# Kernel tuning notes

Hardware: AMD Instinct MI355X
Metric: run time of the kernel (lower is better)

The kernel has to match this reference:

```python
import jax, jax.numpy as jnp
import numpy as np

B, T, D, H, R = 4, 4096, 1024, 16, 256
DH = D // H  # 64


def setup_inputs() -> dict:
    key = jax.random.key(0)
    ks = jax.random.split(key, 5)
    s = 0.02
    return {
        "x": jax.random.normal(ks[0], (B, T, D), dtype=jnp.float32),
        "Wq": jax.random.normal(ks[1], (D, D), dtype=jnp.float32) * s,
        "bq": jnp.zeros((D,), dtype=jnp.float32),
        "Wd": jax.random.normal(ks[2], (D, R), dtype=jnp.float32) * s,
        "bd": jnp.zeros((R,), dtype=jnp.float32),
        "Wu": jax.random.normal(ks[3], (R, 2 * D), dtype=jnp.float32) * s,
        "bu": jnp.zeros((2 * D,), dtype=jnp.float32),
        "Wo": jax.random.normal(ks[4], (D, D), dtype=jnp.float32) * s,
        "bo": jnp.zeros((D,), dtype=jnp.float32),
    }


def reference(x, Wq, bq, Wd, bd, Wu, bu, Wo, bo):
    b, t = x.shape[0], x.shape[1]
    # q projection -> (B,T,H,DH)
    q = (x @ Wq + bq).reshape(b, t, H, DH)
    # low-rank KV: down then up -> (B,T,H,2*DH)
    kv = ((x @ Wd + bd) @ Wu + bu).reshape(b, t, H, 2 * DH)
    k, v = kv[..., :DH], kv[..., DH:]
    # elu+1 feature map
    q = jax.nn.elu(q) + 1.0
    k = jax.nn.elu(k) + 1.0
    # linear attention: context = k^T v per head -> (B,H,DH,DH)
    context = jnp.einsum("bthd,bthe->bhde", k, v)
    out = jnp.einsum("bthd,bhde->bthe", q, context)  # (B,T,H,DH)
    # normalizer: q . sum_t(k)
    k_sum = k.sum(axis=1)  # (B,H,DH)
    z = 1.0 / (jnp.einsum("bthd,bhd->bth", q, k_sum) + 1e-6)
    out = out * z[..., None]
    return out.reshape(b, t, D) @ Wo + bo
```

## Files before the change

### kernel.cpp

```cpp
#include <hip/hip_runtime.h>
#include <hip/hip_bf16.h>
#include <cstddef>
#include <cstdint>

#define B_  4
#define T_  4096
#define D_  1024
#define H_  16
#define DH_ 64
#define R_  256
#define BT_ (B_ * T_)
#define TWO_D_ (2 * D_)

typedef __attribute__((ext_vector_type(8))) short short8;
typedef __attribute__((ext_vector_type(4))) float f32x4;

__device__ __forceinline__ float elu1(float x) {
    return x > 0.0f ? x + 1.0f : __expf(x);
}

__device__ __forceinline__ float bf2f(short u) {
    union { uint32_t i; float f; } c;
    c.i = ((uint32_t)(uint16_t)u) << 16;
    return c.f;
}

typedef __attribute__((address_space(1))) void void_g;
typedef __attribute__((address_space(3))) void void_l;
__device__ __forceinline__ void gld_lds16(const void* g, void* l) {
    __builtin_amdgcn_global_load_lds(
        (const void_g*)(uintptr_t)g,
        (void_l*)(uint32_t)(uintptr_t)l,
        16, 0, 0);
}

__device__ __forceinline__ void store_out(float* p, float v) { *p = v; }
__device__ __forceinline__ void store_out(__hip_bfloat16* p, float v) { *p = __float2bfloat16(v); }

#define PBM 256
#define PBN 256
#define PBK 32

template<int EPI, bool BROW, typename OT>
__global__ __launch_bounds__(512, 2) void gemm_p2(
    const __hip_bfloat16* __restrict__ A,
    const __hip_bfloat16* __restrict__ Bt,
    const float* __restrict__ bias,
    OT* __restrict__ C,
    int M, int N, int K)
{
    __shared__ alignas(16) __hip_bfloat16 sm[2 * 4 * PBM * PBK];
    __hip_bfloat16* Asm = sm;
    __hip_bfloat16* Bsm = sm + 4 * PBM * PBK;

    const int nbx = N / PBN;
    const int nbm = M / PBM;
    const int sh = (nbm < 8) ? nbm : 8;
    const int id = blockIdx.x;
    const int strip = id / (sh * nbx);
    const int wi = id % (sh * nbx);
    const int bm = (strip * sh + (wi % sh)) * PBM;
    const int bn = (wi / sh) * PBN;

    const int tid  = threadIdx.x;
    const int lane = tid & 63;
    const int w    = tid >> 6;
    const int wm   = w >> 2;
    const int wn   = w & 3;
    const int r15  = lane & 15;
    const int kg   = lane >> 4;

    const int c0 = tid, c1 = tid + 512;
    const int rA0 = c0 >> 2, rA1 = c1 >> 2;
    const int gA0 = (c0 & 3) ^ (rA0 & 3), gA1 = (c1 & 3) ^ (rA1 & 3);
    const __hip_bfloat16* a0 = A  + (size_t)(bm + rA0) * K + gA0 * 8;
    const __hip_bfloat16* a1 = A  + (size_t)(bm + rA1) * K + gA1 * 8;
    const __hip_bfloat16* b0 = Bt + (size_t)(bn + rA0) * K + gA0 * 8;
    const __hip_bfloat16* b1 = Bt + (size_t)(bn + rA1) * K + gA1 * 8;

    auto stageA = [&](int t) {
        __hip_bfloat16* d = Asm + (t & 3) * (PBM * PBK);
        gld_lds16(a0 + t * PBK, d + c0 * 8);
        gld_lds16(a1 + t * PBK, d + c1 * 8);
    };
    auto stageB = [&](int t) {
        __hip_bfloat16* d = Bsm + (t & 3) * (PBM * PBK);
        gld_lds16(b0 + t * PBK, d + c0 * 8);
        gld_lds16(b1 + t * PBK, d + c1 * 8);
    };

    const int nk = K / PBK;
    f32x4 acc[8][4] = {};

    stageA(0); stageB(0); stageA(1); stageB(1);

    for (int kt = 0; kt < nk; ++kt) {
        const __hip_bfloat16* As_ = Asm + (kt & 3) * (PBM * PBK);
        const __hip_bfloat16* Bs_ = Bsm + (kt & 3) * (PBM * PBK);

        if (kt + 2 < nk) {
            stageA(kt + 2);
            asm volatile("s_waitcnt vmcnt(6)" ::: "memory");
        } else if (kt + 2 == nk) {
            asm volatile("s_waitcnt vmcnt(4)" ::: "memory");
        } else {
            asm volatile("s_waitcnt vmcnt(0)" ::: "memory");
        }
        __builtin_amdgcn_s_barrier();

        short8 af[8], bf[4];
#pragma unroll
        for (int i = 0; i < 4; ++i) {
            const int r = wm * 128 + i * 16 + r15;
            af[i] = *(const short8*)(As_ + r * PBK + ((kg ^ (r & 3)) * 8));
        }
#pragma unroll
        for (int j = 0; j < 4; ++j) {
            const int r = wn * 64 + j * 16 + r15;
            bf[j] = *(const short8*)(Bs_ + r * PBK + ((kg ^ (r & 3)) * 8));
        }
        __builtin_amdgcn_s_setprio(1);
#pragma unroll
        for (int i = 0; i < 4; ++i)
#pragma unroll
            for (int j = 0; j < 4; ++j)
                acc[i][j] = __builtin_amdgcn_mfma_f32_16x16x32_bf16(af[i], bf[j], acc[i][j], 0, 0, 0);
        __builtin_amdgcn_s_setprio(0);
        __builtin_amdgcn_s_barrier();

        if (kt + 2 < nk) stageB(kt + 2);
#pragma unroll
        for (int i = 4; i < 8; ++i) {
            const int r = wm * 128 + i * 16 + r15;
            af[i] = *(const short8*)(As_ + r * PBK + ((kg ^ (r & 3)) * 8));
        }
        __builtin_amdgcn_s_setprio(1);
#pragma unroll
        for (int i = 4; i < 8; ++i)
#pragma unroll
            for (int j = 0; j < 4; ++j)
                acc[i][j] = __builtin_amdgcn_mfma_f32_16x16x32_bf16(af[i], bf[j], acc[i][j], 0, 0, 0);
        __builtin_amdgcn_s_setprio(0);
        __builtin_amdgcn_s_barrier();
    }

    const int row0 = bm + wm * 128 + (lane >> 4) * 4;

    float brow[8][4];
    if (BROW) {
#pragma unroll
        for (int i = 0; i < 8; ++i)
#pragma unroll
            for (int r = 0; r < 4; ++r) brow[i][r] = bias[row0 + i * 16 + r];
    }
#pragma unroll
    for (int j = 0; j < 4; ++j) {
        const int col = bn + wn * 64 + j * 16 + r15;
        const float bv = BROW ? 0.0f : bias[col];
        const bool kp_col = ((col & 127) < 64);
#pragma unroll
        for (int i = 0; i < 8; ++i) {
#pragma unroll
            for (int r = 0; r < 4; ++r) {
                const int row = row0 + i * 16 + r;
                float v = acc[i][j][r] + (BROW ? brow[i][r] : bv);
                if (EPI == 1) v = elu1(v);
                else if (EPI == 2) {
                    const bool kp = BROW ? ((row & 127) < 64) : kp_col;
                    if (kp) v = elu1(v);
                }
                store_out(C + (size_t)row * N + col, v);
            }
        }
    }
}

#define BM 128
#define BN 128
#define BK 32
#define NBUF 5

template<int EPI, bool BROW, typename OT>
__global__ __launch_bounds__(256) void gemm_bf16(
    const __hip_bfloat16* __restrict__ A,
    const __hip_bfloat16* __restrict__ Bt,
    const float* __restrict__ bias,
    OT* __restrict__ C,
    OT* __restrict__ C2,
    int M, int N, int K)
{
    __shared__ alignas(16) __hip_bfloat16 As[NBUF * BM * BK];
    __shared__ alignas(16) __hip_bfloat16 Bs[NBUF * BN * BK];

    const int nbx = N / BN;
    const int id = blockIdx.x;
    const int strip = id / (8 * nbx);
    const int wi = id % (8 * nbx);
    const int bm = (strip * 8 + (wi & 7)) * BM;
    const int bn = (wi >> 3) * BN;

    const int tid  = threadIdx.x;
    const int lane = tid & 63;
    const int wm   = (tid >> 7) * 64;
    const int wn   = ((tid >> 6) & 1) * 64;
    const int r15  = lane & 15;
    const int kg   = lane >> 4;

    f32x4 acc[4][4] = {};

    const int c0 = tid, c1 = tid + 256;
    const __hip_bfloat16* a0 = A  + (size_t)(bm + (c0 >> 2)) * K + (c0 & 3) * 8;
    const __hip_bfloat16* a1 = A  + (size_t)(bm + (c1 >> 2)) * K + (c1 & 3) * 8;
    const __hip_bfloat16* b0 = Bt + (size_t)(bn + (c0 >> 2)) * K + (c0 & 3) * 8;
    const __hip_bfloat16* b1 = Bt + (size_t)(bn + (c1 >> 2)) * K + (c1 & 3) * 8;

    const int nk = K / BK;

    auto stage = [&](int t) {
        const int buf = t % NBUF;
        __hip_bfloat16* Ad = As + buf * (BM * BK);
        __hip_bfloat16* Bd = Bs + buf * (BN * BK);
        const int k0 = t * BK;
        gld_lds16(a0 + k0, Ad + c0 * 8);
        gld_lds16(a1 + k0, Ad + c1 * 8);
        gld_lds16(b0 + k0, Bd + c0 * 8);
        gld_lds16(b1 + k0, Bd + c1 * 8);
    };

    stage(0); stage(1); stage(2);

    for (int t = 0; t < nk; ++t) {
        if (t + 3 < nk) {
            stage(t + 3);
            asm volatile("s_waitcnt vmcnt(12)\ns_barrier" ::: "memory");
        } else if (t + 2 < nk) {
            asm volatile("s_waitcnt vmcnt(8)\ns_barrier" ::: "memory");
        } else if (t + 1 < nk) {
            asm volatile("s_waitcnt vmcnt(4)\ns_barrier" ::: "memory");
        } else {
            asm volatile("s_waitcnt vmcnt(0)\ns_barrier" ::: "memory");
        }

        const __hip_bfloat16* Asb = As + (t % NBUF) * (BM * BK);
        const __hip_bfloat16* Bsb = Bs + (t % NBUF) * (BN * BK);

        short8 af[4], bf[4];
#pragma unroll
        for (int i = 0; i < 4; ++i) {
            af[i] = *(const short8*)(Asb + (wm + i * 16 + r15) * BK + kg * 8);
            bf[i] = *(const short8*)(Bsb + (wn + i * 16 + r15) * BK + kg * 8);
        }
#pragma unroll
        for (int i = 0; i < 4; ++i)
#pragma unroll
            for (int j = 0; j < 4; ++j)
                acc[i][j] = __builtin_amdgcn_mfma_f32_16x16x32_bf16(af[i], bf[j], acc[i][j], 0, 0, 0);
    }

    const int row0 = bm + wm + (lane >> 4) * 4;

    if (EPI == 3) {
        const bool qreg = (bn < 1024);
#pragma unroll
        for (int j = 0; j < 4; ++j) {
            const int col = bn + wn + j * 16 + r15;
            const float bv = bias[col];
#pragma unroll
            for (int i = 0; i < 4; ++i)
#pragma unroll
                for (int r = 0; r < 4; ++r) {
                    const int row = row0 + i * 16 + r;
                    float v = acc[i][j][r] + bv;
                    if (qreg) {
                        store_out(C + (size_t)row * 1024 + col, elu1(v));
                    } else {
                        store_out(C2 + (size_t)row * 256 + (col - 1024), v);
                    }
                }
        }
        return;
    }

    float brow[4][4];
    if (BROW) {
#pragma unroll
        for (int i = 0; i < 4; ++i)
#pragma unroll
            for (int r = 0; r < 4; ++r) brow[i][r] = bias[row0 + i * 16 + r];
    }
#pragma unroll
    for (int j = 0; j < 4; ++j) {
        const int col = bn + wn + j * 16 + r15;
        const float bv = BROW ? 0.0f : bias[col];
        const bool kp_col = ((col & 127) < 64);
#pragma unroll
        for (int i = 0; i < 4; ++i) {
#pragma unroll
            for (int r = 0; r < 4; ++r) {
                const int row = row0 + i * 16 + r;
                float v = acc[i][j][r] + (BROW ? brow[i][r] : bv);
                if (EPI == 1) v = elu1(v);
                else if (EPI == 2) {
                    const bool kp = BROW ? ((row & 127) < 64) : kp_col;
                    if (kp) v = elu1(v);
                }
                store_out(C + (size_t)row * N + col, v);
            }
        }
    }
}

__global__ __launch_bounds__(256) void cast_bf16_kernel(
    const float* __restrict__ s, __hip_bfloat16* __restrict__ d, int n)
{
    const int i = (blockIdx.x * 256 + threadIdx.x) * 8;
    if (i >= n) return;
    float4 v0 = *(const float4*)(s + i);
    float4 v1 = *(const float4*)(s + i + 4);
    __hip_bfloat16 t[8];
    t[0] = __float2bfloat16(v0.x); t[1] = __float2bfloat16(v0.y);
    t[2] = __float2bfloat16(v0.z); t[3] = __float2bfloat16(v0.w);
    t[4] = __float2bfloat16(v1.x); t[5] = __float2bfloat16(v1.y);
    t[6] = __float2bfloat16(v1.z); t[7] = __float2bfloat16(v1.w);
    *(short8*)(d + i) = *(const short8*)t;
}

__global__ __launch_bounds__(256) void transpose_cast(
    const float* __restrict__ W, __hip_bfloat16* __restrict__ Wt, int K, int N)
{
    __shared__ float t[32][33];
    const int n0 = blockIdx.x * 32, k0 = blockIdx.y * 32;
    const int c = threadIdx.x & 31, r = threadIdx.x >> 5;
#pragma unroll
    for (int rr = r; rr < 32; rr += 8)
        t[rr][c] = W[(size_t)(k0 + rr) * N + n0 + c];
    __syncthreads();
#pragma unroll
    for (int rr = r; rr < 32; rr += 8)
        Wt[(size_t)(n0 + rr) * K + k0 + c] = __float2bfloat16(t[c][rr]);
}

#define CHT 512

__global__ __launch_bounds__(256) void ctx_mfma(
    const __hip_bfloat16* __restrict__ kvT, float* __restrict__ ctx,
    float* __restrict__ ksum)
{
    __shared__ alignas(16) unsigned char smem[40960];
    float* red0 = (float*)smem;
    float* red1 = (float*)(smem + 20480);

    const int bh = blockIdx.x >> 3;
    const int chunk = blockIdx.x & 7;
    const int b = bh >> 4;
    const int h = bh & 15;
    const int tid = threadIdx.x;
    const int lane = tid & 63;
    const int w = tid >> 6;
    const int r15 = lane & 15;
    const int kg  = lane >> 4;

    f32x4 acc[4][4] = {};
    f32x4 acc4[4] = {};

    const short one = (short)0x3F80;
    const short8 bfv = (r15 == 0)
        ? (short8){one, one, one, one, one, one, one, one}
        : (short8){0, 0, 0, 0, 0, 0, 0, 0};

    const size_t tbase = (size_t)b * T_ + (size_t)chunk * CHT;
    const __hip_bfloat16* src = kvT + (size_t)(h * 128) * BT_ + tbase;

    for (int it = 0; it < CHT / 128; ++it) {
#pragma unroll
        for (int r = 0; r < 8; ++r) {
            const int c = r * 256 + tid;
            const int s = c >> 9, j = (c >> 2) & 127, u = c & 3;
            gld_lds16(src + (size_t)j * BT_ + it * 128 + s * 32 + u * 8,
                      smem + c * 16);
        }
        __syncthreads();

        const __hip_bfloat16* Ls = (const __hip_bfloat16*)smem;
        short8 af[4], bf[4];
#pragma unroll
        for (int i = 0; i < 4; ++i) {
            af[i] = *(const short8*)(Ls + (w * 128 + i * 16 + r15) * 32 + kg * 8);
            bf[i] = *(const short8*)(Ls + (w * 128 + 64 + i * 16 + r15) * 32 + kg * 8);
        }
#pragma unroll
        for (int i = 0; i < 4; ++i) {
#pragma unroll
            for (int j = 0; j < 4; ++j)
                acc[i][j] = __builtin_amdgcn_mfma_f32_16x16x32_bf16(af[i], bf[j], acc[i][j], 0, 0, 0);
            acc4[i] = __builtin_amdgcn_mfma_f32_16x16x32_bf16(af[i], bfv, acc4[i], 0, 0, 0);
        }
        __syncthreads();
    }

    const int q4 = lane >> 4;
    auto wr = [&](float* reg) {
#pragma unroll
        for (int i = 0; i < 4; ++i) {
#pragma unroll
            for (int r = 0; r < 4; ++r) {
                const int row = i * 16 + q4 * 4 + r;
#pragma unroll
                for (int j = 0; j < 4; ++j) reg[row * 80 + j * 16 + r15] = acc[i][j][r];
                reg[row * 80 + 64 + r15] = acc4[i][r];
            }
        }
    };
    auto rd = [&](const float* reg) {
#pragma unroll
        for (int i = 0; i < 4; ++i) {
#pragma unroll
            for (int r = 0; r < 4; ++r) {
                const int row = i * 16 + q4 * 4 + r;
#pragma unroll
                for (int j = 0; j < 4; ++j) acc[i][j][r] += reg[row * 80 + j * 16 + r15];
                acc4[i][r] += reg[row * 80 + 64 + r15];
            }
        }
    };

    if (w == 1) wr(red0);
    if (w == 3) wr(red1);
    __syncthreads();
    if (w == 0) rd(red0);
    if (w == 2) rd(red1);
    __syncthreads();
    if (w == 2) wr(red0);
    __syncthreads();
    if (w == 0) { rd(red0); wr(red0); }
    __syncthreads();

    float* cdst = ctx + (size_t)bh * 4096;
#pragma unroll
    for (int r = 0; r < 16; ++r) {
        const int idx = r * 256 + tid;
        const int d = idx >> 6, e = idx & 63;
        atomicAdd(cdst + idx, red0[d * 80 + e]);
    }
    if (tid < 64) atomicAdd(ksum + bh * 64 + tid, red0[tid * 80 + 64]);
}

__global__ __launch_bounds__(256) void pack_ctx(
    const float* __restrict__ ctx, __hip_bfloat16* __restrict__ ctxT)
{
    __shared__ float L[64 * 65];
    const int bh = blockIdx.x;
    const int tid = threadIdx.x;
#pragma unroll
    for (int r = 0; r < 16; ++r) {
        const int idx = r * 256 + tid;
        L[(idx >> 6) * 65 + (idx & 63)] = ctx[(size_t)bh * 4096 + idx];
    }
    __syncthreads();
#pragma unroll
    for (int r = 0; r < 16; ++r) {
        const int idx = r * 256 + tid;
        ctxT[(size_t)bh * 4096 + idx] =
            __float2bfloat16(L[(idx & 63) * 65 + (idx >> 6)]);
    }
}

__global__ __launch_bounds__(256) void out_mfma(
    const __hip_bfloat16* __restrict__ qb, const __hip_bfloat16* __restrict__ ctxT,
    const float* __restrict__ ksum, __hip_bfloat16* __restrict__ outb)
{
    __shared__ alignas(16) unsigned char As[256 * 128];
    __shared__ alignas(16) unsigned char Bs[64 * 128];
    __shared__ float ksumL[64];
    __shared__ float zbuf[256];

    const int bh = blockIdx.x >> 4;
    const int tile = blockIdx.x & 15;
    const int b = bh >> 4;
    const int h = bh & 15;
    const int tid = threadIdx.x;
    const int lane = tid & 63;
    const int w = tid >> 6;
    const int r15 = lane & 15;
    const int kg  = lane >> 4;

    const size_t trow0 = (size_t)b * T_ + (size_t)tile * 256;

#pragma unroll
    for (int r = 0; r < 8; ++r) {
        const int c = r * 256 + tid;
        const int row = c >> 3, slot = c & 7, u = slot ^ (row & 7);
        gld_lds16(qb + (trow0 + row) * D_ + h * 64 + u * 8, As + c * 16);
    }
#pragma unroll
    for (int r = 0; r < 2; ++r) {
        const int c = r * 256 + tid;
        const int row = c >> 3, slot = c & 7, u = slot ^ (row & 7);
        gld_lds16(ctxT + (size_t)bh * 4096 + row * 64 + u * 8, Bs + c * 16);
    }
    if (tid < 64) ksumL[tid] = ksum[bh * 64 + tid];
    __syncthreads();

    short8 af[4][2], bf[4][2];
#pragma unroll
    for (int i = 0; i < 4; ++i)
#pragma unroll
        for (int s = 0; s < 2; ++s) {
            const int m = w * 64 + i * 16 + r15;
            const int n = i * 16 + r15;
            const int uk = s * 4 + kg;
            af[i][s] = *(const short8*)(As + m * 128 + ((uk ^ (m & 7)) * 16));
            bf[i][s] = *(const short8*)(Bs + n * 128 + ((uk ^ (n & 7)) * 16));
        }

    f32x4 acc[4][4] = {};
#pragma unroll
    for (int s = 0; s < 2; ++s)
#pragma unroll
        for (int i = 0; i < 4; ++i)
#pragma unroll
            for (int j = 0; j < 4; ++j)
                acc[i][j] = __builtin_amdgcn_mfma_f32_16x16x32_bf16(af[i][s], bf[j][s], acc[i][j], 0, 0, 0);

    float dsum[4];
#pragma unroll
    for (int i = 0; i < 4; ++i) {
        float s0 = 0.0f;
#pragma unroll
        for (int s = 0; s < 2; ++s)
#pragma unroll
            for (int j8 = 0; j8 < 8; ++j8)
                s0 += bf2f(af[i][s][j8]) * ksumL[s * 32 + kg * 8 + j8];
        s0 += __shfl_xor(s0, 16);
        s0 += __shfl_xor(s0, 32);
        dsum[i] = s0;
    }
    if (lane < 16) {
#pragma unroll
        for (int i = 0; i < 4; ++i)
            zbuf[w * 64 + i * 16 + lane] = 1.0f / (dsum[i] + 1e-6f);
    }
    __syncthreads();

    const int q4 = lane >> 4;
#pragma unroll
    for (int i = 0; i < 4; ++i) {
#pragma unroll
        for (int r = 0; r < 4; ++r) {
            const int m = w * 64 + i * 16 + q4 * 4 + r;
            const float z = zbuf[m];
#pragma unroll
            for (int j = 0; j < 4; ++j) {
                outb[(trow0 + m) * D_ + h * 64 + j * 16 + r15] =
                    __float2bfloat16(acc[i][j][r] * z);
            }
        }
    }
}

extern "C" void kernel_launch(void* const* d_in, const int* in_sizes, int n_in,
                              void* d_out, int out_size, void* d_ws, size_t ws_size,
                              hipStream_t stream) {
    const float* x  = (const float*)d_in[0];
    const float* Wq = (const float*)d_in[1];
    const float* bq = (const float*)d_in[2];
    const float* Wd = (const float*)d_in[3];
    const float* bd = (const float*)d_in[4];
    const float* Wu = (const float*)d_in[5];
    const float* bu = (const float*)d_in[6];
    const float* Wo = (const float*)d_in[7];
    const float* bo = (const float*)d_in[8];
    float* out = (float*)d_out;

    __hip_bfloat16* xb    = (__hip_bfloat16*)d_ws;
    __hip_bfloat16* WqdT  = xb    + (size_t)BT_ * D_;
    __hip_bfloat16* WuT   = WqdT  + (size_t)1280 * D_;
    __hip_bfloat16* WoT   = WuT   + (size_t)TWO_D_ * R_;
    __hip_bfloat16* xdb   = WoT   + (size_t)D_ * D_;
    __hip_bfloat16* kvT   = xdb   + (size_t)BT_ * R_;
    __hip_bfloat16* qb    = kvT   + (size_t)TWO_D_ * BT_;
    float* bias_qd = (float*)(qb + (size_t)BT_ * D_);
    float* ctx  = bias_qd + 1280;
    float* ksum = ctx + (size_t)B_ * H_ * DH_ * DH_;
    __hip_bfloat16* ctxT = (__hip_bfloat16*)(ksum + B_ * H_ * DH_);
    __hip_bfloat16* outb = xb;

    hipMemsetAsync(ctx, 0,
        (size_t)(B_ * H_ * DH_ * DH_ + B_ * H_ * DH_) * sizeof(float), stream);

    cast_bf16_kernel<<<(BT_ * D_) / (8 * 256), 256, 0, stream>>>(x, xb, BT_ * D_);
    transpose_cast<<<dim3(D_ / 32, D_ / 32), 256, 0, stream>>>(Wq, WqdT, D_, D_);
    transpose_cast<<<dim3(R_ / 32, D_ / 32), 256, 0, stream>>>(Wd, WqdT + (size_t)D_ * D_, D_, R_);
    transpose_cast<<<dim3(TWO_D_ / 32, R_ / 32), 256, 0, stream>>>(Wu, WuT, R_, TWO_D_);
    transpose_cast<<<dim3(D_ / 32, D_ / 32), 256, 0, stream>>>(Wo, WoT, D_, D_);

    gemm_bf16<0, false, __hip_bfloat16><<<(BT_ / BM) * (R_ / BN), 256, 0, stream>>>(
        xb, WqdT + (size_t)D_ * D_, bd, xdb, nullptr, BT_, R_, D_);
    gemm_p2<1, false, __hip_bfloat16><<<(BT_ / PBM) * (D_ / PBN), 512, 0, stream>>>(
        xb, WqdT, bq, qb, BT_, D_, D_);
    gemm_p2<2, true, __hip_bfloat16><<<(TWO_D_ / PBM) * (BT_ / PBN), 512, 0, stream>>>(
        WuT, xdb, bu, kvT, TWO_D_, BT_, R_);
    ctx_mfma<<<64 * (T_ / CHT), 256, 0, stream>>>(kvT, ctx, ksum);
    pack_ctx<<<64, 256, 0, stream>>>(ctx, ctxT);
    out_mfma<<<64 * 16, 256, 0, stream>>>(qb, ctxT, ksum, outb);
    gemm_p2<0, false, float><<<(BT_ / PBM) * (D_ / PBN), 512, 0, stream>>>(
        outb, WoT, bo, out, BT_, D_, D_);
}
```

Baseline: 336.1 us.

## Deepen GEMM LDS pipeline to three stages and prefetch next B fragments

```diff
diff --git a/kernel.cpp b/kernel.cpp
--- a/kernel.cpp
+++ b/kernel.cpp
@@ -72,7 +72,7 @@
 
     const int c0 = tid, c1 = tid + 512;
     const int rA0 = c0 >> 2, rA1 = c1 >> 2;
-    const int gA0 = (c0 & 3) ^ (rA0 & 3), gA1 = (c1 & 3) ^ (rA1 & 3);
+    const int gA0 = (c0 & 3) ^ ((rA0 >> 2) & 3), gA1 = (c1 & 3) ^ ((rA1 >> 2) & 3);
     const __hip_bfloat16* a0 = A  + (size_t)(bm + rA0) * K + gA0 * 8;
     const __hip_bfloat16* a1 = A  + (size_t)(bm + rA1) * K + gA1 * 8;
     const __hip_bfloat16* b0 = Bt + (size_t)(bn + rA0) * K + gA0 * 8;
@@ -91,57 +91,74 @@
 
     const int nk = K / PBK;
     f32x4 acc[8][4] = {};
-
-    stageA(0); stageB(0); stageA(1); stageB(1);
-
-    for (int kt = 0; kt < nk; ++kt) {
+    short8 bfA[4], bfB[4];
+
+    stageA(0); stageB(0); stageA(1); stageB(1); stageA(2); stageB(2);
+    asm volatile("s_waitcnt vmcnt(8)" ::: "memory");
+    __builtin_amdgcn_s_barrier();
+#pragma unroll
+    for (int j = 0; j < 4; ++j) {
+        const int r = wn * 64 + j * 16 + r15;
+        bfA[j] = *(const short8*)(Bsm + r * PBK + ((kg ^ ((r >> 2) & 3)) * 8));
+    }
+
+    auto step = [&](int kt, short8 (&bfc)[4], short8 (&bfn)[4]) {
         const __hip_bfloat16* As_ = Asm + (kt & 3) * (PBM * PBK);
-        const __hip_bfloat16* Bs_ = Bsm + (kt & 3) * (PBM * PBK);
-
-        if (kt + 2 < nk) {
-            stageA(kt + 2);
+        const __hip_bfloat16* Bn_ = Bsm + ((kt + 1) & 3) * (PBM * PBK);
+        short8 af0[4], af1[4];
+
+        if (kt + 3 < nk) stageA(kt + 3);
+#pragma unroll
+        for (int i = 0; i < 4; ++i) {
+            const int r = wm * 128 + i * 16 + r15;
+            af0[i] = *(const short8*)(As_ + r * PBK + ((kg ^ ((r >> 2) & 3)) * 8));
+        }
+#pragma unroll
+        for (int i = 0; i < 4; ++i) {
+            const int r = wm * 128 + 64 + i * 16 + r15;
+            af1[i] = *(const short8*)(As_ + r * PBK + ((kg ^ ((r >> 2) & 3)) * 8));
+        }
+        asm volatile("s_waitcnt lgkmcnt(4)" ::: "memory");
+        if (kt + 3 < nk) {
             asm volatile("s_waitcnt vmcnt(6)" ::: "memory");
-        } else if (kt + 2 == nk) {
+        } else if (kt + 2 < nk) {
             asm volatile("s_waitcnt vmcnt(4)" ::: "memory");
+        } else if (kt + 1 < nk) {
+            asm volatile("s_waitcnt vmcnt(0)" ::: "memory");
+        }
+        __builtin_amdgcn_s_barrier();
+        __builtin_amdgcn_s_setprio(1);
+#pragma unroll
+        for (int i = 0; i < 4; ++i)
+#pragma unroll
+            for (int j = 0; j < 4; ++j)
+                acc[i][j] = __builtin_amdgcn_mfma_f32_16x16x32_bf16(af0[i], bfc[j], acc[i][j], 0, 0, 0);
+        __builtin_amdgcn_s_setprio(0);
+
+        if (kt + 3 < nk) stageB(kt + 3);
+        if (kt + 1 < nk) {
+#pragma unroll
+            for (int j = 0; j < 4; ++j) {
+                const int r = wn * 64 + j * 16 + r15;
+                bfn[j] = *(const short8*)(Bn_ + r * PBK + ((kg ^ ((r >> 2) & 3)) * 8));
+            }
+            asm volatile("s_waitcnt lgkmcnt(4)" ::: "memory");
         } else {
-            asm volatile("s_waitcnt vmcnt(0)" ::: "memory");
+            asm volatile("s_waitcnt lgkmcnt(0)" ::: "memory");
         }
         __builtin_amdgcn_s_barrier();
-
-        short8 af[8], bf[4];
-#pragma unroll
-        for (int i = 0; i < 4; ++i) {
-            const int r = wm * 128 + i * 16 + r15;
-            af[i] = *(const short8*)(As_ + r * PBK + ((kg ^ (r & 3)) * 8));
-        }
-#pragma unroll
-        for (int j = 0; j < 4; ++j) {
-            const int r = wn * 64 + j * 16 + r15;
-            bf[j] = *(const short8*)(Bs_ + r * PBK + ((kg ^ (r & 3)) * 8));
-        }
         __builtin_amdgcn_s_setprio(1);
 #pragma unroll
         for (int i = 0; i < 4; ++i)
 #pragma unroll
             for (int j = 0; j < 4; ++j)
-                acc[i][j] = __builtin_amdgcn_mfma_f32_16x16x32_bf16(af[i], bf[j], acc[i][j], 0, 0, 0);
+                acc[4 + i][j] = __builtin_amdgcn_mfma_f32_16x16x32_bf16(af1[i], bfc[j], acc[4 + i][j], 0, 0, 0);
         __builtin_amdgcn_s_setprio(0);
-        __builtin_amdgcn_s_barrier();
-
-        if (kt + 2 < nk) stageB(kt + 2);
-#pragma unroll
-        for (int i = 4; i < 8; ++i) {
-            const int r = wm * 128 + i * 16 + r15;
-            af[i] = *(const short8*)(As_ + r * PBK + ((kg ^ (r & 3)) * 8));
-        }
-        __builtin_amdgcn_s_setprio(1);
-#pragma unroll
-        for (int i = 4; i < 8; ++i)
-#pragma unroll
-            for (int j = 0; j < 4; ++j)
-                acc[i][j] = __builtin_amdgcn_mfma_f32_16x16x32_bf16(af[i], bf[j], acc[i][j], 0, 0, 0);
-        __builtin_amdgcn_s_setprio(0);
-        __builtin_amdgcn_s_barrier();
+    };
+
+    for (int kt = 0; kt < nk; kt += 2) {
+        step(kt,     bfA, bfB);
+        step(kt + 1, bfB, bfA);
     }
 
     const int row0 = bm + wm * 128 + (lane >> 4) * 4;
```

After: 333.0 us. About the same (-0.9%).

## Rewrite 256x256 GEMM mainloop with BK=64 and 8-phase interleaved pipeline

Applied to the files above, without the earlier changes.

```diff
diff --git a/kernel.cpp b/kernel.cpp
--- a/kernel.cpp
+++ b/kernel.cpp
@@ -39,27 +39,25 @@
 
 #define PBM 256
 #define PBN 256
-#define PBK 32
 
 template<int EPI, bool BROW, typename OT>
-__global__ __launch_bounds__(512, 2) void gemm_p2(
+__global__ __launch_bounds__(512, 2) void gemm_p8(
     const __hip_bfloat16* __restrict__ A,
     const __hip_bfloat16* __restrict__ Bt,
     const float* __restrict__ bias,
     OT* __restrict__ C,
     int M, int N, int K)
 {
-    __shared__ alignas(16) __hip_bfloat16 sm[2 * 4 * PBM * PBK];
+    __shared__ alignas(16) __hip_bfloat16 sm[65536];
     __hip_bfloat16* Asm = sm;
-    __hip_bfloat16* Bsm = sm + 4 * PBM * PBK;
+    __hip_bfloat16* Bsm = sm + 32768;
 
     const int nbx = N / PBN;
     const int nbm = M / PBM;
     const int sh = (nbm < 8) ? nbm : 8;
     const int id = blockIdx.x;
-    const int strip = id / (sh * nbx);
     const int wi = id % (sh * nbx);
-    const int bm = (strip * sh + (wi % sh)) * PBM;
+    const int bm = ((id / (sh * nbx)) * sh + (wi % sh)) * PBM;
     const int bn = (wi / sh) * PBN;
 
     const int tid  = threadIdx.x;
@@ -70,79 +68,207 @@
     const int r15  = lane & 15;
     const int kg   = lane >> 4;
 
-    const int c0 = tid, c1 = tid + 512;
-    const int rA0 = c0 >> 2, rA1 = c1 >> 2;
-    const int gA0 = (c0 & 3) ^ (rA0 & 3), gA1 = (c1 & 3) ^ (rA1 & 3);
-    const __hip_bfloat16* a0 = A  + (size_t)(bm + rA0) * K + gA0 * 8;
-    const __hip_bfloat16* a1 = A  + (size_t)(bm + rA1) * K + gA1 * 8;
-    const __hip_bfloat16* b0 = Bt + (size_t)(bn + rA0) * K + gA0 * 8;
-    const __hip_bfloat16* b1 = Bt + (size_t)(bn + rA1) * K + gA1 * 8;
-
-    auto stageA = [&](int t) {
-        __hip_bfloat16* d = Asm + (t & 3) * (PBM * PBK);
-        gld_lds16(a0 + t * PBK, d + c0 * 8);
-        gld_lds16(a1 + t * PBK, d + c1 * 8);
+    const int nt = K / 64;
+
+    const int rl = tid >> 3;
+    const int g  = (tid & 7) ^ (rl & 7);
+    const __hip_bfloat16* aS = A  + (size_t)(bm + rl) * K + g * 8;
+    const __hip_bfloat16* bS = Bt + (size_t)(bn + rl) * K + g * 8;
+    __hip_bfloat16* dA = Asm + tid * 8;
+    __hip_bfloat16* dB = Bsm + tid * 8;
+
+    auto stA = [&](int t, int h) {
+        const int tc = (t < nt) ? t : (nt - 1);
+        __hip_bfloat16* d = dA + ((t & 1) * 2 + h) * 8192;
+        const __hip_bfloat16* s = aS + (size_t)(h * 128) * K + tc * 64;
+        gld_lds16(s, d);
+        gld_lds16(s + (size_t)64 * K, d + 4096);
     };
-    auto stageB = [&](int t) {
-        __hip_bfloat16* d = Bsm + (t & 3) * (PBM * PBK);
-        gld_lds16(b0 + t * PBK, d + c0 * 8);
-        gld_lds16(b1 + t * PBK, d + c1 * 8);
+    auto stB = [&](int t, int h) {
+        const int tc = (t < nt) ? t : (nt - 1);
+        __hip_bfloat16* d = dB + ((t & 1) * 2 + h) * 8192;
+        const __hip_bfloat16* s = bS + (size_t)(h * 128) * K + tc * 64;
+        gld_lds16(s, d);
+        gld_lds16(s + (size_t)64 * K, d + 4096);
     };
 
-    const int nk = K / PBK;
+    const int x3    = (r15 & 7) << 3;
+    const int kofs0 = (kg * 8) ^ x3;
+    const int kofs1 = (32 + kg * 8) ^ x3;
+    const __hip_bfloat16* Af0 = Asm + wm * 8192 + r15 * 64;
+    const __hip_bfloat16* Bf0 = Bsm + (wn >> 1) * 8192 + (wn & 1) * 4096 + r15 * 64;
+    const __hip_bfloat16* Af1 = Af0 + 16384;
+    const __hip_bfloat16* Bf1 = Bf0 + 16384;
+
     f32x4 acc[8][4] = {};
-
-    stageA(0); stageB(0); stageA(1); stageB(1);
-
-    for (int kt = 0; kt < nk; ++kt) {
-        const __hip_bfloat16* As_ = Asm + (kt & 3) * (PBM * PBK);
-        const __hip_bfloat16* Bs_ = Bsm + (kt & 3) * (PBM * PBK);
-
-        if (kt + 2 < nk) {
-            stageA(kt + 2);
-            asm volatile("s_waitcnt vmcnt(6)" ::: "memory");
-        } else if (kt + 2 == nk) {
-            asm volatile("s_waitcnt vmcnt(4)" ::: "memory");
-        } else {
-            asm volatile("s_waitcnt vmcnt(0)" ::: "memory");
-        }
-        __builtin_amdgcn_s_barrier();
-
-        short8 af[8], bf[4];
+    short8 af[8][2], bf[4][2];
+
+    stA(0, 0); stA(0, 1); stB(0, 0); stB(0, 1); stA(1, 0); stA(1, 1);
+    asm volatile("s_waitcnt vmcnt(4)" ::: "memory");
+    __builtin_amdgcn_s_barrier();
+
+    for (int t = 0; t < nt; t += 2) {
 #pragma unroll
         for (int i = 0; i < 4; ++i) {
-            const int r = wm * 128 + i * 16 + r15;
-            af[i] = *(const short8*)(As_ + r * PBK + ((kg ^ (r & 3)) * 8));
-        }
-#pragma unroll
-        for (int j = 0; j < 4; ++j) {
-            const int r = wn * 64 + j * 16 + r15;
-            bf[j] = *(const short8*)(Bs_ + r * PBK + ((kg ^ (r & 3)) * 8));
-        }
+            af[i][0] = *(const short8*)(Af0 + i * 1024 + kofs0);
+            af[i][1] = *(const short8*)(Af0 + i * 1024 + kofs1);
+        }
+#pragma unroll
+        for (int j = 0; j < 2; ++j) {
+            bf[j][0] = *(const short8*)(Bf0 + j * 1024 + kofs0);
+            bf[j][1] = *(const short8*)(Bf0 + j * 1024 + kofs1);
+        }
+        stB(t + 1, 0);
+        __builtin_amdgcn_s_barrier();
+        asm volatile("s_waitcnt lgkmcnt(0)" ::: "memory");
+        __builtin_amdgcn_sched_barrier(0);
         __builtin_amdgcn_s_setprio(1);
 #pragma unroll
         for (int i = 0; i < 4; ++i)
 #pragma unroll
-            for (int j = 0; j < 4; ++j)
-                acc[i][j] = __builtin_amdgcn_mfma_f32_16x16x32_bf16(af[i], bf[j], acc[i][j], 0, 0, 0);
+            for (int j = 0; j < 2; ++j) {
+                acc[i][j] = __builtin_amdgcn_mfma_f32_16x16x32_bf16(af[i][0], bf[j][0], acc[i][j], 0, 0, 0);
+                acc[i][j] = __builtin_amdgcn_mfma_f32_16x16x32_bf16(af[i][1], bf[j][1], acc[i][j], 0, 0, 0);
+            }
         __builtin_amdgcn_s_setprio(0);
         __builtin_amdgcn_s_barrier();
 
-        if (kt + 2 < nk) stageB(kt + 2);
 #pragma unroll
         for (int i = 4; i < 8; ++i) {
-            const int r = wm * 128 + i * 16 + r15;
-            af[i] = *(const short8*)(As_ + r * PBK + ((kg ^ (r & 3)) * 8));
-        }
+            af[i][0] = *(const short8*)(Af0 + i * 1024 + kofs0);
+            af[i][1] = *(const short8*)(Af0 + i * 1024 + kofs1);
+        }
+        stB(t + 1, 1);
+        __builtin_amdgcn_s_barrier();
+        asm volatile("s_waitcnt lgkmcnt(0)" ::: "memory");
+        __builtin_amdgcn_sched_barrier(0);
         __builtin_amdgcn_s_setprio(1);
 #pragma unroll
         for (int i = 4; i < 8; ++i)
 #pragma unroll
-            for (int j = 0; j < 4; ++j)
-                acc[i][j] = __builtin_amdgcn_mfma_f32_16x16x32_bf16(af[i], bf[j], acc[i][j], 0, 0, 0);
+            for (int j = 0; j < 2; ++j) {
+                acc[i][j] = __builtin_amdgcn_mfma_f32_16x16x32_bf16(af[i][0], bf[j][0], acc[i][j], 0, 0, 0);
+                acc[i][j] = __builtin_amdgcn_mfma_f32_16x16x32_bf16(af[i][1], bf[j][1], acc[i][j], 0, 0, 0);
+            }
         __builtin_amdgcn_s_setprio(0);
         __builtin_amdgcn_s_barrier();
-    }
+
+#pragma unroll
+        for (int j = 2; j < 4; ++j) {
+            bf[j][0] = *(const short8*)(Bf0 + j * 1024 + kofs0);
+            bf[j][1] = *(const short8*)(Bf0 + j * 1024 + kofs1);
+        }
+        stA(t + 2, 0);
+        __builtin_amdgcn_s_barrier();
+        asm volatile("s_waitcnt lgkmcnt(0)" ::: "memory");
+        __builtin_amdgcn_sched_barrier(0);
+        __builtin_amdgcn_s_setprio(1);
+#pragma unroll
+        for (int i = 4; i < 8; ++i)
+#pragma unroll
+            for (int j = 2; j < 4; ++j) {
+                acc[i][j] = __builtin_amdgcn_mfma_f32_16x16x32_bf16(af[i][0], bf[j][0], acc[i][j], 0, 0, 0);
+                acc[i][j] = __builtin_amdgcn_mfma_f32_16x16x32_bf16(af[i][1], bf[j][1], acc[i][j], 0, 0, 0);
+            }
+        __builtin_amdgcn_s_setprio(0);
+        __builtin_amdgcn_s_barrier();
+
+        stA(t + 2, 1);
+        asm volatile("s_waitcnt vmcnt(4)" ::: "memory");
+        __builtin_amdgcn_s_barrier();
+        __builtin_amdgcn_sched_barrier(0);
+        __builtin_amdgcn_s_setprio(1);
+#pragma unroll
+        for (int i = 0; i < 4; ++i)
+#pragma unroll
+            for (int j = 2; j < 4; ++j) {
+                acc[i][j] = __builtin_amdgcn_mfma_f32_16x16x32_bf16(af[i][0], bf[j][0], acc[i][j], 0, 0, 0);
+                acc[i][j] = __builtin_amdgcn_mfma_f32_16x16x32_bf16(af[i][1], bf[j][1], acc[i][j], 0, 0, 0);
+            }
+        __builtin_amdgcn_s_setprio(0);
+        __builtin_amdgcn_s_barrier();
+
+#pragma unroll
+        for (int i = 0; i < 4; ++i) {
+            af[i][0] = *(const short8*)(Af1 + i * 1024 + kofs0);
+            af[i][1] = *(const short8*)(Af1 + i * 1024 + kofs1);
+        }
+#pragma unroll
+        for (int j = 0; j < 2; ++j) {
+            bf[j][0] = *(const short8*)(Bf1 + j * 1024 + kofs0);
+            bf[j][1] = *(const short8*)(Bf1 + j * 1024 + kofs1);
+        }
+        stB(t + 2, 0);
+        __builtin_amdgcn_s_barrier();
+        asm volatile("s_waitcnt lgkmcnt(0)" ::: "memory");
+        __builtin_amdgcn_sched_barrier(0);
+        __builtin_amdgcn_s_setprio(1);
+#pragma unroll
+        for (int i = 0; i < 4; ++i)
+#pragma unroll
+            for (int j = 0; j < 2; ++j) {
+                acc[i][j] = __builtin_amdgcn_mfma_f32_16x16x32_bf16(af[i][0], bf[j][0], acc[i][j], 0, 0, 0);
+                acc[i][j] = __builtin_amdgcn_mfma_f32_16x16x32_bf16(af[i][1], bf[j][1], acc[i][j], 0, 0, 0);
+            }
+        __builtin_amdgcn_s_setprio(0);
+        __builtin_amdgcn_s_barrier();
+
+#pragma unroll
+        for (int i = 4; i < 8; ++i) {
+            af[i][0] = *(const short8*)(Af1 + i * 1024 + kofs0);
+            af[i][1] = *(const short8*)(Af1 + i * 1024 + kofs1);
+        }
+        stB(t + 2, 1);
+        __builtin_amdgcn_s_barrier();
+        asm volatile("s_waitcnt lgkmcnt(0)" ::: "memory");
+        __builtin_amdgcn_sched_barrier(0);
+        __builtin_amdgcn_s_setprio(1);
+#pragma unroll
+        for (int i = 4; i < 8; ++i)
+#pragma unroll
+            for (int j = 0; j < 2; ++j) {
+                acc[i][j] = __builtin_amdgcn_mfma_f32_16x16x32_bf16(af[i][0], bf[j][0], acc[i][j], 0, 0, 0);
+                acc[i][j] = __builtin_amdgcn_mfma_f32_16x16x32_bf16(af[i][1], bf[j][1], acc[i][j], 0, 0, 0);
+            }
+        __builtin_amdgcn_s_setprio(0);
+        __builtin_amdgcn_s_barrier();
+
+#pragma unroll
+        for (int j = 2; j < 4; ++j) {
+            bf[j][0] = *(const short8*)(Bf1 + j * 1024 + kofs0);
+            bf[j][1] = *(const short8*)(Bf1 + j * 1024 + kofs1);
+        }
+        stA(t + 3, 0);
+        __builtin_amdgcn_s_barrier();
+        asm volatile("s_waitcnt lgkmcnt(0)" ::: "memory");
+        __builtin_amdgcn_sched_barrier(0);
+        __builtin_amdgcn_s_setprio(1);
+#pragma unroll
+        for (int i = 4; i < 8; ++i)
+#pragma unroll
+            for (int j = 2; j < 4; ++j) {
+                acc[i][j] = __builtin_amdgcn_mfma_f32_16x16x32_bf16(af[i][0], bf[j][0], acc[i][j], 0, 0, 0);
+                acc[i][j] = __builtin_amdgcn_mfma_f32_16x16x32_bf16(af[i][1], bf[j][1], acc[i][j], 0, 0, 0);
+            }
+        __builtin_amdgcn_s_setprio(0);
+        __builtin_amdgcn_s_barrier();
+
+        stA(t + 3, 1);
+        asm volatile("s_waitcnt vmcnt(4)" ::: "memory");
+        __builtin_amdgcn_s_barrier();
+        __builtin_amdgcn_sched_barrier(0);
+        __builtin_amdgcn_s_setprio(1);
+#pragma unroll
+        for (int i = 0; i < 4; ++i)
+#pragma unroll
+            for (int j = 2; j < 4; ++j) {
+                acc[i][j] = __builtin_amdgcn_mfma_f32_16x16x32_bf16(af[i][0], bf[j][0], acc[i][j], 0, 0, 0);
+                acc[i][j] = __builtin_amdgcn_mfma_f32_16x16x32_bf16(af[i][1], bf[j][1], acc[i][j], 0, 0, 0);
+            }
+        __builtin_amdgcn_s_setprio(0);
+        __builtin_amdgcn_s_barrier();
+    }
+    asm volatile("s_waitcnt vmcnt(0)" ::: "memory");
 
     const int row0 = bm + wm * 128 + (lane >> 4) * 4;
 
@@ -596,13 +722,13 @@
 
     gemm_bf16<0, false, __hip_bfloat16><<<(BT_ / BM) * (R_ / BN), 256, 0, stream>>>(
         xb, WqdT + (size_t)D_ * D_, bd, xdb, nullptr, BT_, R_, D_);
-    gemm_p2<1, false, __hip_bfloat16><<<(BT_ / PBM) * (D_ / PBN), 512, 0, stream>>>(
+    gemm_p8<1, false, __hip_bfloat16><<<(BT_ / PBM) * (D_ / PBN), 512, 0, stream>>>(
         xb, WqdT, bq, qb, BT_, D_, D_);
-    gemm_p2<2, true, __hip_bfloat16><<<(TWO_D_ / PBM) * (BT_ / PBN), 512, 0, stream>>>(
+    gemm_p8<2, true, __hip_bfloat16><<<(TWO_D_ / PBM) * (BT_ / PBN), 512, 0, stream>>>(
         WuT, xdb, bu, kvT, TWO_D_, BT_, R_);
     ctx_mfma<<<64 * (T_ / CHT), 256, 0, stream>>>(kvT, ctx, ksum);
     pack_ctx<<<64, 256, 0, stream>>>(ctx, ctxT);
     out_mfma<<<64 * 16, 256, 0, stream>>>(qb, ctxT, ksum, outb);
-    gemm_p2<0, false, float><<<(BT_ / PBM) * (D_ / PBN), 512, 0, stream>>>(
+    gemm_p8<0, false, float><<<(BT_ / PBM) * (D_ / PBN), 512, 0, stream>>>(
         outb, WoT, bo, out, BT_, D_, D_);
 }
```

Measured after the change: 326.5 us. 1.03x faster.
